# Performance work log

Hardware: AMD Instinct MI355X
Metric: run time of the kernel (lower is better)

The kernel has to match this reference:

```python
import jax, jax.numpy as jnp
import numpy as np

S, B, H = 2048, 1, 1024
N_HEADS = 16
HEAD_DIM = H // N_HEADS
E, K, F = 8, 2, 2048  # experts, top_k, ffn_hidden
EPS = 1e-5


def layernorm(x, w, b):
    mu = jnp.mean(x, axis=-1, keepdims=True)
    var = jnp.mean(jnp.square(x - mu), axis=-1, keepdims=True)
    return (x - mu) * jax.lax.rsqrt(var + EPS) * w + b


def setup_inputs() -> dict:
    key = jax.random.key(0)
    ks = jax.random.split(key, 8)
    std = 0.02
    return {
        "x": jax.random.normal(ks[0], (S, B, H), dtype=jnp.float32),
        "ln1_w": jnp.ones((H,), jnp.float32),
        "ln1_b": jnp.zeros((H,), jnp.float32),
        "in_proj_w": jax.random.normal(ks[1], (3 * H, H), jnp.float32) * std,
        "in_proj_b": jnp.zeros((3 * H,), jnp.float32),
        "out_proj_w": jax.random.normal(ks[2], (H, H), jnp.float32) * std,
        "out_proj_b": jnp.zeros((H,), jnp.float32),
        "ln2_w": jnp.ones((H,), jnp.float32),
        "ln2_b": jnp.zeros((H,), jnp.float32),
        "router_w": jax.random.normal(ks[3], (E, H), jnp.float32) * std,
        "w1": jax.random.normal(ks[4], (E, H, F), jnp.float32) * std,
        "w2": jax.random.normal(ks[5], (E, F, H), jnp.float32) * std,
    }


def reference(x, ln1_w, ln1_b, in_proj_w, in_proj_b, out_proj_w, out_proj_b,
              ln2_w, ln2_b, router_w, w1, w2):
    s, b, h = x.shape
    # ---- causal self-attention (nn.MultiheadAttention math) ----
    hn = layernorm(x, ln1_w, ln1_b)
    qkv = hn @ in_proj_w.T + in_proj_b          # [S,B,3H]
    q, k, v = jnp.split(qkv, 3, axis=-1)
    q = q.reshape(s, b, N_HEADS, HEAD_DIM)
    k = k.reshape(s, b, N_HEADS, HEAD_DIM)
    v = v.reshape(s, b, N_HEADS, HEAD_DIM)
    scores = jnp.einsum('sbnd,tbnd->bnst', q, k) / np.sqrt(HEAD_DIM)
    causal = jnp.tril(jnp.ones((s, s), bool))
    scores = jnp.where(causal[None, None], scores, -jnp.inf)
    probs = jax.nn.softmax(scores, axis=-1)
    attn = jnp.einsum('bnst,tbnd->sbnd', probs, v).reshape(s, b, h)
    attn = attn @ out_proj_w.T + out_proj_b
    x1 = x + attn
    # ---- dMoE FFN: router softmax -> top-k gates -> expert GELU MLP ----
    hn2 = layernorm(x1, ln2_w, ln2_b).reshape(s * b, h)   # tokens [T,H]
    logits = hn2 @ router_w.T                              # [T,E]
    rp = jax.nn.softmax(logits, axis=-1)
    topw, topi = jax.lax.top_k(rp, K)                      # [T,K]
    gates = jnp.sum(jax.nn.one_hot(topi, E, dtype=hn2.dtype) * topw[..., None], axis=1)  # [T,E]
    hmid = jax.nn.gelu(jnp.einsum('th,ehf->tef', hn2, w1), approximate=False)  # [T,E,F]
    y = jnp.einsum('tef,efh->th', hmid * gates[:, :, None], w2)                # [T,H]
    return x1 + y.reshape(s, b, h)
```

## Files before the change

### kernel.cpp

```cpp
#include <hip/hip_runtime.h>

#define SL 2048
#define HID 1024
#define NHEAD 16
#define HD 64
#define NEXP 8
#define FF 2048
#define MAXTILE 40
#define MAXROWS (MAXTILE * 128)
#define CPAD 32

typedef short bf16x8 __attribute__((ext_vector_type(8)));
typedef float f32x4 __attribute__((ext_vector_type(4)));
typedef unsigned u32x4 __attribute__((ext_vector_type(4)));

__device__ __forceinline__ unsigned short f2bf(float f) {
  unsigned u = __builtin_bit_cast(unsigned, f);
  u += 0x7fffu + ((u >> 16) & 1u);
  return (unsigned short)(u >> 16);
}

__device__ __forceinline__ void gload16(const void* g, void* l) {
  __builtin_amdgcn_global_load_lds((const __attribute__((address_space(1))) void*)g,
                                   (__attribute__((address_space(3))) void*)l,
                                   16, 0, 0);
}

__device__ __forceinline__ void xcd_remap(int& bx, int& by) {
  const int nx = gridDim.x;
  const int nwg = nx * gridDim.y;
  const int L = by * nx + bx;
  const int per = nwg >> 3;
  const int Lp = (L & 7) * per + (L >> 3);
  bx = Lp % nx;
  by = Lp / nx;
}

struct TransLds { float Afp[64 * 128]; unsigned Bu[128 * 33]; };

__device__ __forceinline__ void trans_tile(
    int tile, const float* __restrict__ w1, const float* __restrict__ w2,
    unsigned short* __restrict__ w1t, unsigned short* __restrict__ w2t,
    int tid, TransLds* T)
{
  const int m = tile >> 8;
  const int t = tile & 255;
  const float* in;
  unsigned short* out;
  int R, C, r0, c0;
  if (m < 8) {
    in = w1 + (size_t)m * HID * FF;  out = w1t + (size_t)m * HID * FF;
    R = HID; C = FF;  r0 = (t >> 4) * 64;  c0 = (t & 15) * 128;
  } else {
    in = w2 + (size_t)(m - 8) * FF * HID;  out = w2t + (size_t)(m - 8) * FF * HID;
    R = FF; C = HID;  r0 = (t >> 3) * 64;  c0 = (t & 7) * 128;
  }
  const int wv = tid >> 6, ln = tid & 63;
#pragma unroll
  for (int p = 0; p < 8; p++) {
    const int ebase = p * 1024 + wv * 256;
    const int eo = ebase + ln * 4;
    const int r = eo >> 7, c = eo & 127;
    gload16(in + (size_t)(r0 + r) * C + c0 + c, (char*)T->Afp + (size_t)ebase * 4);
  }
  asm volatile("s_waitcnt vmcnt(0)" ::: "memory");
  __syncthreads();
#pragma unroll
  for (int it = 0; it < 16; it++) {
    const int idx = it * 256 + tid;
    const int rp = idx >> 7;
    const int c = idx & 127;
    const float v0 = T->Afp[(2 * rp) * 128 + c];
    const float v1 = T->Afp[(2 * rp + 1) * 128 + c];
    T->Bu[c * 33 + rp] = (unsigned)f2bf(v0) | ((unsigned)f2bf(v1) << 16);
  }
  __syncthreads();
#pragma unroll
  for (int it = 0; it < 8; it++) {
    const int idx = it * 256 + tid;
    const int c = idx >> 4;
    const int r4 = (idx & 15) * 4;
    const unsigned u0 = T->Bu[c * 33 + (r4 >> 1)];
    const unsigned u1 = T->Bu[c * 33 + (r4 >> 1) + 1];
    ushort4 u;
    u.x = (unsigned short)(u0 & 0xffff);
    u.y = (unsigned short)(u0 >> 16);
    u.z = (unsigned short)(u1 & 0xffff);
    u.w = (unsigned short)(u1 >> 16);
    *reinterpret_cast<ushort4*>(&out[(size_t)(c0 + c) * R + r0 + r4]) = u;
  }
}

#define PIPE_WAIT(i, NT)                                                     \
  if ((i) == (NT) - 1)                                                       \
    asm volatile("s_waitcnt vmcnt(0) lgkmcnt(0)" ::: "memory");              \
  else                                                                       \
    asm volatile("s_waitcnt vmcnt(4) lgkmcnt(0)" ::: "memory");              \
  __builtin_amdgcn_s_barrier();

#define GEMM_FRAGS_MFMA(CC)                                                  \
  bf16x8 af[4], bfr[4];                                                      \
  _Pragma("unroll")                                                          \
  for (int mt = 0; mt < 4; mt++)                                             \
    af[mt] = *reinterpret_cast<const bf16x8*>(                               \
        &Asm[CC][(wm + mt * 16 + la) * 32 + lk]);                            \
  _Pragma("unroll")                                                          \
  for (int nt = 0; nt < 4; nt++)                                             \
    bfr[nt] = *reinterpret_cast<const bf16x8*>(                              \
        &Bsm[CC][(wn + nt * 16 + la) * 32 + lk]);                            \
  __builtin_amdgcn_s_setprio(1);                                             \
  _Pragma("unroll")                                                          \
  for (int mt = 0; mt < 4; mt++)                                             \
    _Pragma("unroll")                                                        \
    for (int nt = 0; nt < 4; nt++)                                           \
      acc[mt][nt] =                                                          \
          __builtin_amdgcn_mfma_f32_16x16x32_bf16(af[mt], bfr[nt], acc[mt][nt], 0, 0, 0); \
  __builtin_amdgcn_s_setprio(0);

#define PIPE_ROT()                                                           \
  cc = (cc == 2) ? 0 : cc + 1;                                               \
  cs = (cs == 2) ? 0 : cs + 1;

__global__ __launch_bounds__(256) void qkv_trans_kernel(
    const unsigned short* __restrict__ A, const unsigned short* __restrict__ Bt,
    const float* __restrict__ bias,
    unsigned short* __restrict__ q_out, unsigned short* __restrict__ k_out,
    unsigned short* __restrict__ vt_out,
    const float* __restrict__ w1, const float* __restrict__ w2,
    unsigned short* __restrict__ w1t, unsigned short* __restrict__ w2t)
{
  __shared__ union {
    struct { unsigned short A[3][4096]; unsigned short B[3][4096]; } g;
    TransLds t;
  } sm;
  const int tid = threadIdx.x;

  if (blockIdx.z == 0) {
    unsigned short (*Asm)[4096] = sm.g.A;
    unsigned short (*Bsm)[4096] = sm.g.B;
    int bx = blockIdx.x, by = blockIdx.y;
    xcd_remap(bx, by);
    const int wave = tid >> 6;
    const int lane = tid & 63;
    const int m0 = by * 128;
    const int n0 = bx * 128;
    const int wm = (wave >> 1) * 64;
    const int wn = (wave & 1) * 64;
    const int la = lane & 15;
    const int lk = (lane >> 4) * 8;

    f32x4 acc[4][4] = {};

    const int srow = tid >> 2;
    const int skoff = (tid & 3) * 8;
    const unsigned short* Ag = A + (size_t)(m0 + srow) * HID + skoff;
    const unsigned short* Bg = Bt + (size_t)(n0 + srow) * HID + skoff;

    auto stage = [&](int s, int k0) {
      gload16(Ag + k0, &Asm[s][wave * 512]);
      gload16(Ag + (size_t)64 * HID + k0, &Asm[s][2048 + wave * 512]);
      gload16(Bg + k0, &Bsm[s][wave * 512]);
      gload16(Bg + (size_t)64 * HID + k0, &Bsm[s][2048 + wave * 512]);
    };

    stage(0, 0);
    stage(1, 32);
    const int NT = HID >> 5;
    int cc = 0, cs = 2;
    for (int i = 0; i < NT; ++i) {
      PIPE_WAIT(i, NT)
      if (i + 2 < NT) stage(cs, (i + 2) << 5);
      GEMM_FRAGS_MFMA(cc)
      PIPE_ROT()
    }

    const int lg = lane >> 4;
#pragma unroll
    for (int mt = 0; mt < 4; mt++) {
#pragma unroll
      for (int nt = 0; nt < 4; nt++) {
#pragma unroll
        for (int r = 0; r < 4; r++) {
          const int row = m0 + wm + mt * 16 + lg * 4 + r;
          const int col = n0 + wn + nt * 16 + la;
          float v = acc[mt][nt][r] + bias[col];
          const int hh = (col & 1023) >> 6;
          const int dd = col & 63;
          const unsigned short bv = f2bf(v);
          if (col < 1024)
            q_out[(size_t)hh * SL * HD + (size_t)row * HD + dd] = bv;
          else if (col < 2048)
            k_out[(size_t)hh * SL * HD + (size_t)row * HD + dd] = bv;
          else
            vt_out[(size_t)hh * HD * SL + (size_t)dd * SL + row] = bv;
        }
      }
    }
  } else {
    const int id = blockIdx.y * 24 + blockIdx.x;
    const int tile = 512 + ((int)blockIdx.z - 1) * 384 + id;
    trans_tile(tile, w1, w2, w1t, w2t, tid, &sm.t);
  }
}

__global__ __launch_bounds__(256) void gemm_bt2(
    const unsigned short* __restrict__ A, const unsigned short* __restrict__ Bt,
    float* __restrict__ outf,
    const float* __restrict__ w1, const float* __restrict__ w2,
    unsigned short* __restrict__ w1t, unsigned short* __restrict__ w2t)
{
  __shared__ union {
    struct { unsigned short A[3][4096]; unsigned short B[3][4096]; } g;
    TransLds t;
  } sm;
  const int tid = threadIdx.x;

  if (blockIdx.z >= 2) {
    const int id = blockIdx.y * 8 + blockIdx.x;
    const int tile = 3200 + ((int)blockIdx.z - 2) * 128 + id;
    trans_tile(tile, w1, w2, w1t, w2t, tid, &sm.t);
    return;
  }

  unsigned short (*Asm)[4096] = sm.g.A;
  unsigned short (*Bsm)[4096] = sm.g.B;
  int bx = blockIdx.x, by = blockIdx.y;
  xcd_remap(bx, by);
  const int wave = tid >> 6;
  const int lane = tid & 63;
  const int m0 = by * 128;
  const int n0 = bx * 128;
  const int koff = blockIdx.z * (HID / 2);
  const int wm = (wave >> 1) * 64;
  const int wn = (wave & 1) * 64;
  const int la = lane & 15;
  const int lk = (lane >> 4) * 8;

  f32x4 acc[4][4] = {};

  const int srow = tid >> 2;
  const int skoff = (tid & 3) * 8;
  const unsigned short* Ag = A + (size_t)(m0 + srow) * HID + koff + skoff;
  const unsigned short* Bg = Bt + (size_t)(n0 + srow) * HID + koff + skoff;

  auto stage = [&](int s, int k0) {
    gload16(Ag + k0, &Asm[s][wave * 512]);
    gload16(Ag + (size_t)64 * HID + k0, &Asm[s][2048 + wave * 512]);
    gload16(Bg + k0, &Bsm[s][wave * 512]);
    gload16(Bg + (size_t)64 * HID + k0, &Bsm[s][2048 + wave * 512]);
  };

  stage(0, 0);
  stage(1, 32);
  const int NT = (HID / 2) >> 5;
  int cc = 0, cs = 2;
  for (int i = 0; i < NT; ++i) {
    PIPE_WAIT(i, NT)
    if (i + 2 < NT) stage(cs, (i + 2) << 5);
    GEMM_FRAGS_MFMA(cc)
    PIPE_ROT()
  }

  const int lg = lane >> 4;
#pragma unroll
  for (int mt = 0; mt < 4; mt++) {
#pragma unroll
    for (int nt = 0; nt < 4; nt++) {
#pragma unroll
      for (int r = 0; r < 4; r++) {
        const int row = m0 + wm + mt * 16 + lg * 4 + r;
        const int col = n0 + wn + nt * 16 + la;
        outf[(size_t)blockIdx.z * SL * HID + (size_t)row * HID + col] = acc[mt][nt][r];
      }
    }
  }
}

__global__ __launch_bounds__(256) void gemm_moe1(
    const unsigned short* __restrict__ A, const unsigned short* __restrict__ w1t,
    const int* __restrict__ perm, const float* __restrict__ gateg,
    const int* __restrict__ texp, const int* __restrict__ trow,
    unsigned short* __restrict__ hmidg)
{
  __shared__ unsigned short Asm[3][128 * 32];
  __shared__ unsigned short Bsm[3][128 * 32];
  int bx = blockIdx.x, by = blockIdx.y;
  xcd_remap(bx, by);
  const int e = texp[by];
  if (e < 0) return;
  const int row0 = trow[by];
  const int tid = threadIdx.x;
  const int wave = tid >> 6;
  const int lane = tid & 63;
  const int n0 = bx * 128;
  const int wm = (wave >> 1) * 64;
  const int wn = (wave & 1) * 64;
  const int la = lane & 15;
  const int lk = (lane >> 4) * 8;
  f32x4 acc[4][4] = {};

  const int srow = tid >> 2;
  const int skoff = (tid & 3) * 8;
  const int p0 = perm[row0 + srow];
  const int p1 = perm[row0 + 64 + srow];
  const unsigned short* Ag0 = A + (size_t)(p0 < 0 ? 0 : (p0 >> 1)) * HID + skoff;
  const unsigned short* Ag1 = A + (size_t)(p1 < 0 ? 0 : (p1 >> 1)) * HID + skoff;
  const unsigned short* Bg = w1t + (size_t)e * HID * FF + (size_t)(n0 + srow) * HID + skoff;

  auto stage = [&](int s, int k0) {
    gload16(Ag0 + k0, &Asm[s][wave * 512]);
    gload16(Ag1 + k0, &Asm[s][2048 + wave * 512]);
    gload16(Bg + k0, &Bsm[s][wave * 512]);
    gload16(Bg + (size_t)64 * HID + k0, &Bsm[s][2048 + wave * 512]);
  };

  stage(0, 0);
  stage(1, 32);
  const int NT = HID >> 5;
  int cc = 0, cs = 2;
  for (int i = 0; i < NT; ++i) {
    PIPE_WAIT(i, NT)
    if (i + 2 < NT) stage(cs, (i + 2) << 5);
    GEMM_FRAGS_MFMA(cc)
    PIPE_ROT()
  }

  const int lg = lane >> 4;
#pragma unroll
  for (int mt = 0; mt < 4; mt++) {
    float gr[4];
#pragma unroll
    for (int r = 0; r < 4; r++) gr[r] = gateg[row0 + wm + mt * 16 + lg * 4 + r];
#pragma unroll
    for (int nt = 0; nt < 4; nt++) {
#pragma unroll
      for (int r = 0; r < 4; r++) {
        const int grow = row0 + wm + mt * 16 + lg * 4 + r;
        const int col = n0 + wn + nt * 16 + la;
        const float v = acc[mt][nt][r];
        const float g = 0.5f * v * (1.0f + erff(v * 0.70710678118f));
        hmidg[(size_t)grow * FF + col] = f2bf(g * gr[r]);
      }
    }
  }
}

__global__ __launch_bounds__(256) void gemm_moe2(
    const unsigned short* __restrict__ A, const unsigned short* __restrict__ w2t,
    const int* __restrict__ perm,
    const int* __restrict__ texp, const int* __restrict__ trow,
    float* __restrict__ ybuf)
{
  __shared__ unsigned short Asm[3][128 * 32];
  __shared__ unsigned short Bsm[3][128 * 32];
  int bx = blockIdx.x, by = blockIdx.y;
  xcd_remap(bx, by);
  const int e = texp[by];
  if (e < 0) return;
  const int row0 = trow[by];
  const int tid = threadIdx.x;
  const int wave = tid >> 6;
  const int lane = tid & 63;
  const int n0 = bx * 128;
  const int koff = blockIdx.z * (FF / 2);
  const int wm = (wave >> 1) * 64;
  const int wn = (wave & 1) * 64;
  const int la = lane & 15;
  const int lk = (lane >> 4) * 8;
  f32x4 acc[4][4] = {};

  const int srow = tid >> 2;
  const int skoff = (tid & 3) * 8;
  const unsigned short* Ag = A + (size_t)(row0 + srow) * FF + koff + skoff;
  const unsigned short* Bg = w2t + (size_t)e * FF * HID + (size_t)(n0 + srow) * FF + koff + skoff;

  auto stage = [&](int s, int k0) {
    gload16(Ag + k0, &Asm[s][wave * 512]);
    gload16(Ag + (size_t)64 * FF + k0, &Asm[s][2048 + wave * 512]);
    gload16(Bg + k0, &Bsm[s][wave * 512]);
    gload16(Bg + (size_t)64 * FF + k0, &Bsm[s][2048 + wave * 512]);
  };

  stage(0, 0);
  stage(1, 32);
  const int NT = (FF / 2) >> 5;
  int cc = 0, cs = 2;
  for (int i = 0; i < NT; ++i) {
    PIPE_WAIT(i, NT)
    if (i + 2 < NT) stage(cs, (i + 2) << 5);
    GEMM_FRAGS_MFMA(cc)
    PIPE_ROT()
  }

  const int lg = lane >> 4;
#pragma unroll
  for (int mt = 0; mt < 4; mt++) {
    int pr[4];
#pragma unroll
    for (int r = 0; r < 4; r++) pr[r] = perm[row0 + wm + mt * 16 + lg * 4 + r];
#pragma unroll
    for (int nt = 0; nt < 4; nt++) {
#pragma unroll
      for (int r = 0; r < 4; r++) {
        const int p = pr[r];
        if (p >= 0) {
          const int col = n0 + wn + nt * 16 + la;
          ybuf[(size_t)(blockIdx.z * 2 + (p & 1)) * SL * HID + (size_t)(p >> 1) * HID + col] =
              acc[mt][nt][r];
        }
      }
    }
  }
}

__global__ __launch_bounds__(256) void ln_conv_kernel(
    const float* __restrict__ x, const float* __restrict__ w, const float* __restrict__ b,
    unsigned short* __restrict__ ob,
    const float4* __restrict__ cva, const float4* __restrict__ cvb,
    ushort4* __restrict__ coa, ushort4* __restrict__ cob,
    const float* __restrict__ w1, const float* __restrict__ w2,
    unsigned short* __restrict__ w1t, unsigned short* __restrict__ w2t)
{
  __shared__ union { struct { float ps[4], pq[4]; } l; TransLds t; } sm;
  const int tid = threadIdx.x;
  if ((int)blockIdx.x < SL) {
    const int row = blockIdx.x;
    const float4 v = *reinterpret_cast<const float4*>(&x[(size_t)row * HID + tid * 4]);
    float s = v.x + v.y + v.z + v.w;
    float q = v.x * v.x + v.y * v.y + v.z * v.z + v.w * v.w;
    for (int off = 32; off > 0; off >>= 1) {
      s += __shfl_down(s, off);
      q += __shfl_down(q, off);
    }
    const int wave = tid >> 6, lane = tid & 63;
    if (lane == 0) { sm.l.ps[wave] = s; sm.l.pq[wave] = q; }
    __syncthreads();
    s = sm.l.ps[0] + sm.l.ps[1] + sm.l.ps[2] + sm.l.ps[3];
    q = sm.l.pq[0] + sm.l.pq[1] + sm.l.pq[2] + sm.l.pq[3];
    const float mu = s * (1.0f / HID);
    const float inv = rsqrtf(q * (1.0f / HID) - mu * mu + 1e-5f);
    const int i = tid * 4;
    const float4 wv = *reinterpret_cast<const float4*>(&w[i]);
    const float4 bv = *reinterpret_cast<const float4*>(&b[i]);
    ushort4 u;
    u.x = f2bf((v.x - mu) * inv * wv.x + bv.x);
    u.y = f2bf((v.y - mu) * inv * wv.y + bv.y);
    u.z = f2bf((v.z - mu) * inv * wv.z + bv.z);
    u.w = f2bf((v.w - mu) * inv * wv.w + bv.w);
    *reinterpret_cast<ushort4*>(&ob[(size_t)row * HID + i]) = u;
  } else if ((int)blockIdx.x < SL + 512) {
    const int NA = 3 * HID * HID / 4, NB = HID * HID / 4;
    for (int i = ((int)blockIdx.x - SL) * 256 + tid; i < NA + NB; i += 512 * 256) {
      if (i < NA) {
        const float4 v = cva[i];
        ushort4 u; u.x = f2bf(v.x); u.y = f2bf(v.y); u.z = f2bf(v.z); u.w = f2bf(v.w);
        coa[i] = u;
      } else {
        const float4 v = cvb[i - NA];
        ushort4 u; u.x = f2bf(v.x); u.y = f2bf(v.y); u.z = f2bf(v.z); u.w = f2bf(v.w);
        cob[i - NA] = u;
      }
    }
  } else {
    const int tile = (int)blockIdx.x - SL - 512;
    trans_tile(tile, w1, w2, w1t, w2t, tid, &sm.t);
  }
}

__global__ __launch_bounds__(256) void combine_ln(
    const float4* __restrict__ x, const float* __restrict__ bias,
    const float4* __restrict__ p0, const float4* __restrict__ p1,
    float4* __restrict__ x1,
    const float* __restrict__ w, const float* __restrict__ b,
    unsigned short* __restrict__ ob,
    const float* __restrict__ rw,
    int* __restrict__ ti, float* __restrict__ tg, int* __restrict__ cnt)
{
  __shared__ float ps[4], pq[4];
  __shared__ float rsm[4][8];
  const int row = blockIdx.x;
  const int tid = threadIdx.x;
  const int i4 = row * 256 + tid;
  const int i = tid * 4;
  const float4 bv0 = *reinterpret_cast<const float4*>(&bias[i]);
  const float4 a = x[i4], c = p0[i4], d = p1[i4];
  float4 v;
  v.x = a.x + bv0.x + c.x + d.x;
  v.y = a.y + bv0.y + c.y + d.y;
  v.z = a.z + bv0.z + c.z + d.z;
  v.w = a.w + bv0.w + c.w + d.w;
  x1[i4] = v;
  float s = v.x + v.y + v.z + v.w;
  float q = v.x * v.x + v.y * v.y + v.z * v.z + v.w * v.w;
  for (int off = 32; off > 0; off >>= 1) {
    s += __shfl_down(s, off);
    q += __shfl_down(q, off);
  }
  const int wave = tid >> 6, lane = tid & 63;
  if (lane == 0) { ps[wave] = s; pq[wave] = q; }
  __syncthreads();
  s = ps[0] + ps[1] + ps[2] + ps[3];
  q = pq[0] + pq[1] + pq[2] + pq[3];
  const float mu = s * (1.0f / HID);
  const float inv = rsqrtf(q * (1.0f / HID) - mu * mu + 1e-5f);
  const float4 wv = *reinterpret_cast<const float4*>(&w[i]);
  const float4 bv = *reinterpret_cast<const float4*>(&b[i]);
  const float o0 = (v.x - mu) * inv * wv.x + bv.x;
  const float o1 = (v.y - mu) * inv * wv.y + bv.y;
  const float o2 = (v.z - mu) * inv * wv.z + bv.z;
  const float o3 = (v.w - mu) * inv * wv.w + bv.w;
  ushort4 u; u.x = f2bf(o0); u.y = f2bf(o1); u.z = f2bf(o2); u.w = f2bf(o3);
  *reinterpret_cast<ushort4*>(&ob[(size_t)row * HID + i]) = u;

  float pl[NEXP];
#pragma unroll
  for (int e = 0; e < NEXP; e++) {
    const float4 rv = *reinterpret_cast<const float4*>(&rw[e * HID + i]);
    pl[e] = o0 * rv.x + o1 * rv.y + o2 * rv.z + o3 * rv.w;
  }
#pragma unroll
  for (int e = 0; e < NEXP; e++) {
    pl[e] += __shfl_xor(pl[e], 32);
    pl[e] += __shfl_xor(pl[e], 16);
    pl[e] += __shfl_xor(pl[e], 8);
    pl[e] += __shfl_xor(pl[e], 4);
    pl[e] += __shfl_xor(pl[e], 2);
    pl[e] += __shfl_xor(pl[e], 1);
  }
  if (lane == 0) {
#pragma unroll
    for (int e = 0; e < NEXP; e++) rsm[wave][e] = pl[e];
  }
  __syncthreads();
  if (tid == 0) {
    float lgt[NEXP];
#pragma unroll
    for (int e = 0; e < NEXP; e++)
      lgt[e] = rsm[0][e] + rsm[1][e] + rsm[2][e] + rsm[3][e];
    float mx = lgt[0];
#pragma unroll
    for (int e = 1; e < NEXP; e++) mx = fmaxf(mx, lgt[e]);
    float Z = 0.f;
    float pexp[NEXP];
#pragma unroll
    for (int e = 0; e < NEXP; e++) { pexp[e] = expf(lgt[e] - mx); Z += pexp[e]; }
    const float invZ = 1.f / Z;
    int i1 = 0;
#pragma unroll
    for (int e = 1; e < NEXP; e++) if (pexp[e] > pexp[i1]) i1 = e;
    int i2 = (i1 == 0) ? 1 : 0;
#pragma unroll
    for (int e = 0; e < NEXP; e++) if (e != i1 && pexp[e] > pexp[i2]) i2 = e;
    ti[2 * row] = i1; ti[2 * row + 1] = i2;
    tg[2 * row] = pexp[i1] * invZ; tg[2 * row + 1] = pexp[i2] * invZ;
    atomicAdd(&cnt[i1 * CPAD], 1);
    atomicAdd(&cnt[i2 * CPAD], 1);
  }
}

__global__ __launch_bounds__(256) void scan_build_kernel(
    const int* __restrict__ cnt, const int* __restrict__ ti, const float* __restrict__ tg,
    int* __restrict__ texp, int* __restrict__ trow,
    int* __restrict__ perm, float* __restrict__ gateg)
{
  __shared__ int poff[NEXP];
  __shared__ int lfill[NEXP];
  const int tid = threadIdx.x;
  if (tid == 0) {
    int off = 0, nt = 0;
    for (int e = 0; e < NEXP; e++) {
      poff[e] = off;
      const int c = cnt[e * CPAD];
      const int ntl = (c + 127) >> 7;
      for (int i = 0; i < ntl; i++) { texp[nt] = e; trow[nt] = off + i * 128; nt++; }
      off += ntl * 128;
    }
    for (int i = nt; i < MAXTILE; i++) { texp[i] = -1; trow[i] = 0; }
  }
  if (tid < NEXP) lfill[tid] = 0;
  __syncthreads();
  for (int t = tid; t < SL; t += 256) {
#pragma unroll
    for (int s2 = 0; s2 < 2; s2++) {
      const int e = ti[2 * t + s2];
      const int l = atomicAdd(&lfill[e], 1);
      const int pos = poff[e] + l;
      perm[pos] = 2 * t + s2;
      gateg[pos] = tg[2 * t + s2];
    }
  }
}

__global__ __launch_bounds__(256) void final_add(
    const float4* __restrict__ x1, const float4* __restrict__ y0,
    const float4* __restrict__ y1, const float4* __restrict__ y2,
    const float4* __restrict__ y3, float4* __restrict__ out)
{
  const int i = blockIdx.x * 256 + threadIdx.x;
  const float4 a = x1[i], b = y0[i], c = y1[i], d = y2[i], e = y3[i];
  float4 o;
  o.x = a.x + b.x + c.x + d.x + e.x;
  o.y = a.y + b.y + c.y + d.y + e.y;
  o.z = a.z + b.z + c.z + d.z + e.z;
  o.w = a.w + b.w + c.w + d.w + e.w;
  out[i] = o;
}

#define SC2 0.1803368801111204f
#define PPITCH 20
__global__ __launch_bounds__(512) void attn_kernel(
    const unsigned short* __restrict__ qb, const unsigned short* __restrict__ kb,
    const unsigned short* __restrict__ vtb, unsigned short* __restrict__ attn)
{
  const int h = blockIdx.y;
  const int tid = threadIdx.x;
  const int wave = tid >> 6, lane = tid & 63;
  const int grp = wave >> 2;
  const int w4 = wave & 3;
  const int la = lane & 15, lg = lane >> 4;
  const int la7 = la & 7;
  __shared__ unsigned short Kt[2][2][64 * 64];
  __shared__ unsigned short Vt[2][2][64 * 64];
  __shared__ unsigned plds[8 * 32 * PPITCH];
  const unsigned short* qh = qb + (size_t)h * SL * HD;
  const unsigned short* kh = kb + (size_t)h * SL * HD;
  const unsigned short* vh = vtb + (size_t)h * HD * SL;
  unsigned* pu = &plds[wave * 32 * PPITCH];

  const int sr_lo = w4 * 8 + (lane >> 3);
  const int ss = lane & 7;

  auto stageKV = [&](int t, int buf) {
    const int kvb = t * 64;
#pragma unroll
    for (int j = 0; j < 2; j++) {
      const int row = j * 32 + sr_lo;
      const int s = ss ^ (row & 7);
      gload16(kh + (size_t)(kvb + row) * HD + s * 8, &Kt[grp][buf][j * 2048 + w4 * 512]);
      gload16(vh + (size_t)row * SL + kvb + s * 8, &Vt[grp][buf][j * 2048 + w4 * 512]);
    }
  };

  for (int half = 0; half < 2; half++) {
    const int qt = half ? (31 - blockIdx.x) : blockIdx.x;
    const int m0 = qt * 64 + w4 * 16;
    const int T = qt + 1;
    const int S = (T + 1) >> 1;
    const int q = m0 + la;

    bf16x8 aq0 = *reinterpret_cast<const bf16x8*>(&qh[(size_t)(m0 + la) * HD + lg * 8]);
    bf16x8 aq1 = *reinterpret_cast<const bf16x8*>(&qh[(size_t)(m0 + la) * HD + 32 + lg * 8]);

    f32x4 oacc[4] = {};
    float mrun = -1e30f, lrun = 0.f;

    if (grp < T) stageKV(grp, 0);
    __syncthreads();
    int cur = 0;

    for (int s = 0; s < S; s++) {
      const int tmy = 2 * s + grp;
      if (tmy + 2 < T) stageKV(tmy + 2, cur ^ 1);
      if (tmy < T) {
        const int kv0 = tmy * 64;
        const unsigned short* Kb = Kt[grp][cur];
        const unsigned short* Vb = Vt[grp][cur];

        f32x4 sac[4] = {};
        __builtin_amdgcn_s_setprio(1);
#pragma unroll
        for (int nt = 0; nt < 4; nt++) {
          const int row = nt * 16 + la;
          bf16x8 b0 = *reinterpret_cast<const bf16x8*>(&Kb[row * 64 + ((lg ^ la7) << 3)]);
          bf16x8 b1 = *reinterpret_cast<const bf16x8*>(&Kb[row * 64 + (((4 + lg) ^ la7) << 3)]);
          sac[nt] = __builtin_amdgcn_mfma_f32_16x16x32_bf16(b0, aq0, sac[nt], 0, 0, 0);
          sac[nt] = __builtin_amdgcn_mfma_f32_16x16x32_bf16(b1, aq1, sac[nt], 0, 0, 0);
        }
        __builtin_amdgcn_s_setprio(0);
        float sv[4][4];
        const bool diag = (tmy == qt);
#pragma unroll
        for (int nt = 0; nt < 4; nt++)
#pragma unroll
          for (int r = 0; r < 4; r++) {
            float xs = sac[nt][r] * SC2;
            if (diag && (kv0 + nt * 16 + lg * 4 + r) > q) xs = -1e30f;
            sv[nt][r] = xs;
          }
        float pm = fmaxf(fmaxf(sv[0][0], sv[0][1]), fmaxf(sv[0][2], sv[0][3]));
#pragma unroll
        for (int nt = 1; nt < 4; nt++)
          pm = fmaxf(pm, fmaxf(fmaxf(sv[nt][0], sv[nt][1]), fmaxf(sv[nt][2], sv[nt][3])));
        pm = fmaxf(pm, __shfl_xor(pm, 16));
        pm = fmaxf(pm, __shfl_xor(pm, 32));
        const float mn = fmaxf(mrun, pm);
        float rs = 0.f;
#pragma unroll
        for (int nt = 0; nt < 4; nt++)
#pragma unroll
          for (int r = 0; r < 4; r++) {
            const float pe = exp2f(sv[nt][r] - mn);
            sv[nt][r] = pe;
            rs += pe;
          }
        rs += __shfl_xor(rs, 16);
        rs += __shfl_xor(rs, 32);
        if (__ballot(pm > mrun) != 0ULL) {
          const float al = exp2f(mrun - mn);
#pragma unroll
          for (int dt = 0; dt < 4; dt++)
#pragma unroll
            for (int r = 0; r < 4; r++) oacc[dt][r] *= al;
          lrun = lrun * al + rs;
          mrun = mn;
        } else {
          lrun += rs;
        }
#pragma unroll
        for (int nt = 0; nt < 4; nt++)
#pragma unroll
          for (int rp = 0; rp < 2; rp++) {
            unsigned pk;
            asm("v_cvt_pk_bf16_f32 %0, %1, %2"
                : "=v"(pk) : "v"(sv[nt][rp * 2]), "v"(sv[nt][rp * 2 + 1]));
            pu[(nt * 8 + lg * 2 + rp) * PPITCH + la] = pk;
          }
        asm volatile("s_waitcnt lgkmcnt(0)" ::: "memory");
        __builtin_amdgcn_sched_barrier(0);
        u32x4 w0, w1;
#pragma unroll
        for (int jj = 0; jj < 4; jj++) {
          w0[jj] = pu[(lg * 4 + jj) * PPITCH + la];
          w1[jj] = pu[(16 + lg * 4 + jj) * PPITCH + la];
        }
        const bf16x8 pa0 = __builtin_bit_cast(bf16x8, w0);
        const bf16x8 pa1 = __builtin_bit_cast(bf16x8, w1);
        __builtin_amdgcn_s_setprio(1);
#pragma unroll
        for (int dt = 0; dt < 4; dt++) {
          const int row = dt * 16 + la;
          bf16x8 v0 = *reinterpret_cast<const bf16x8*>(&Vb[row * 64 + ((lg ^ la7) << 3)]);
          bf16x8 v1 = *reinterpret_cast<const bf16x8*>(&Vb[row * 64 + (((4 + lg) ^ la7) << 3)]);
          oacc[dt] = __builtin_amdgcn_mfma_f32_16x16x32_bf16(v0, pa0, oacc[dt], 0, 0, 0);
          oacc[dt] = __builtin_amdgcn_mfma_f32_16x16x32_bf16(v1, pa1, oacc[dt], 0, 0, 0);
        }
        __builtin_amdgcn_s_setprio(0);
      }
      __syncthreads();
      cur ^= 1;
    }

    float* xb = (float*)&Kt[0][0][0];
    float* mlb = (float*)&Vt[0][0][0];
    if (grp == 1) {
#pragma unroll
      for (int dt = 0; dt < 4; dt++)
#pragma unroll
        for (int r = 0; r < 4; r++)
          xb[w4 * 1024 + (dt * 16 + lg * 4 + r) * 16 + la] = oacc[dt][r];
      if (lg == 0) {
        mlb[w4 * 32 + la * 2] = mrun;
        mlb[w4 * 32 + la * 2 + 1] = lrun;
      }
    }
    __syncthreads();
    if (grp == 0) {
      const float m1 = mlb[w4 * 32 + la * 2];
      const float l1 = mlb[w4 * 32 + la * 2 + 1];
      const float mm = fmaxf(mrun, m1);
      const float a0 = exp2f(mrun - mm);
      const float a1 = exp2f(m1 - mm);
      const float linv = 1.0f / (lrun * a0 + l1 * a1);
#pragma unroll
      for (int dt = 0; dt < 4; dt++) {
        ushort4 u;
        float o0 = (oacc[dt][0] * a0 + xb[w4 * 1024 + (dt * 16 + lg * 4 + 0) * 16 + la] * a1) * linv;
        float o1 = (oacc[dt][1] * a0 + xb[w4 * 1024 + (dt * 16 + lg * 4 + 1) * 16 + la] * a1) * linv;
        float o2 = (oacc[dt][2] * a0 + xb[w4 * 1024 + (dt * 16 + lg * 4 + 2) * 16 + la] * a1) * linv;
        float o3 = (oacc[dt][3] * a0 + xb[w4 * 1024 + (dt * 16 + lg * 4 + 3) * 16 + la] * a1) * linv;
        u.x = f2bf(o0); u.y = f2bf(o1); u.z = f2bf(o2); u.w = f2bf(o3);
        *reinterpret_cast<ushort4*>(&attn[(size_t)q * HID + h * HD + dt * 16 + lg * 4]) = u;
      }
    }
    __syncthreads();
  }
}

extern "C" void kernel_launch(void* const* d_in, const int* in_sizes, int n_in,
                              void* d_out, int out_size, void* d_ws, size_t ws_size,
                              hipStream_t stream)
{
  const float* x          = (const float*)d_in[0];
  const float* ln1_w      = (const float*)d_in[1];
  const float* ln1_b      = (const float*)d_in[2];
  const float* in_proj_w  = (const float*)d_in[3];
  const float* in_proj_b  = (const float*)d_in[4];
  const float* out_proj_w = (const float*)d_in[5];
  const float* out_proj_b = (const float*)d_in[6];
  const float* ln2_w      = (const float*)d_in[7];
  const float* ln2_b      = (const float*)d_in[8];
  const float* router_w   = (const float*)d_in[9];
  const float* w1         = (const float*)d_in[10];
  const float* w2         = (const float*)d_in[11];
  float* out = (float*)d_out;

  char* ws = (char*)d_ws;
  size_t off = 0;
  auto alloc = [&](size_t bytes) -> void* {
    void* p = ws + off;
    off += (bytes + 255) & ~(size_t)255;
    return p;
  };
  unsigned short* hn_b   = (unsigned short*)alloc((size_t)SL * HID * 2);
  unsigned short* ipw_b  = (unsigned short*)alloc((size_t)3 * HID * HID * 2);
  unsigned short* opw_b  = (unsigned short*)alloc((size_t)HID * HID * 2);
  unsigned short* qb     = (unsigned short*)alloc((size_t)SL * HID * 2);
  unsigned short* kb     = (unsigned short*)alloc((size_t)SL * HID * 2);
  unsigned short* vtb    = (unsigned short*)alloc((size_t)SL * HID * 2);
  unsigned short* attn_b = (unsigned short*)alloc((size_t)SL * HID * 2);
  float*          x1     = (float*)alloc((size_t)SL * HID * 4);
  float*          pbuf   = (float*)alloc((size_t)2 * SL * HID * 4);
  unsigned short* hn2_b  = (unsigned short*)alloc((size_t)SL * HID * 2);
  unsigned short* w1t    = (unsigned short*)alloc((size_t)NEXP * HID * FF * 2);
  unsigned short* w2t    = (unsigned short*)alloc((size_t)NEXP * HID * FF * 2);
  unsigned short* hmidg  = (unsigned short*)alloc((size_t)MAXROWS * FF * 2);
  float*          ybuf   = (float*)alloc((size_t)4 * SL * HID * 4);
  int*            ti     = (int*)alloc((size_t)SL * 2 * 4);
  float*          tg     = (float*)alloc((size_t)SL * 2 * 4);
  int*            perm   = (int*)alloc((size_t)MAXROWS * 4);
  float*          gateg  = (float*)alloc((size_t)MAXROWS * 4);
  int*            cnt    = (int*)alloc(NEXP * CPAD * 4);
  int*            poff   = (int*)alloc(64 * 4);
  int*            texp   = (int*)alloc(64 * 4);
  int*            trow   = (int*)alloc(64 * 4);
  (void)poff;

  const dim3 blk(256);

  hipMemsetAsync(cnt, 0, NEXP * CPAD * 4, stream);
  hipMemsetAsync(perm, 0xFF, (size_t)MAXROWS * 4, stream);
  hipMemsetAsync(gateg, 0, (size_t)MAXROWS * 4, stream);

  ln_conv_kernel<<<SL + 1024, blk, 0, stream>>>(
      x, ln1_w, ln1_b, hn_b,
      (const float4*)in_proj_w, (const float4*)out_proj_w,
      (ushort4*)ipw_b, (ushort4*)opw_b,
      w1, w2, w1t, w2t);

  qkv_trans_kernel<<<dim3(3 * HID / 128, SL / 128, 8), blk, 0, stream>>>(
      hn_b, ipw_b, in_proj_b, qb, kb, vtb, w1, w2, w1t, w2t);

  attn_kernel<<<dim3(16, NHEAD), dim3(512), 0, stream>>>(qb, kb, vtb, attn_b);

  gemm_bt2<<<dim3(HID / 128, SL / 128, 9), blk, 0, stream>>>(
      attn_b, opw_b, pbuf, w1, w2, w1t, w2t);

  combine_ln<<<SL, blk, 0, stream>>>(
      (const float4*)x, out_proj_b, (const float4*)pbuf,
      (const float4*)(pbuf + (size_t)SL * HID), (float4*)x1,
      ln2_w, ln2_b, hn2_b,
      router_w, ti, tg, cnt);

  scan_build_kernel<<<1, blk, 0, stream>>>(cnt, ti, tg, texp, trow, perm, gateg);

  gemm_moe1<<<dim3(FF / 128, MAXTILE), blk, 0, stream>>>(
      hn2_b, w1t, perm, gateg, texp, trow, hmidg);
  gemm_moe2<<<dim3(HID / 128, MAXTILE, 2), blk, 0, stream>>>(
      hmidg, w2t, perm, texp, trow, ybuf);

  final_add<<<SL * HID / 1024, blk, 0, stream>>>(
      (const float4*)x1, (const float4*)ybuf,
      (const float4*)(ybuf + (size_t)SL * HID),
      (const float4*)(ybuf + (size_t)2 * SL * HID),
      (const float4*)(ybuf + (size_t)3 * SL * HID),
      (float4*)out);
}
```

Before: 244.8 us.

## Fuse scan into combine_ln via last-block pattern and atomically accumulate MoE output

```diff
diff --git a/kernel.cpp b/kernel.cpp
--- a/kernel.cpp
+++ b/kernel.cpp
@@ -349,7 +349,7 @@
     const unsigned short* __restrict__ A, const unsigned short* __restrict__ w2t,
     const int* __restrict__ perm,
     const int* __restrict__ texp, const int* __restrict__ trow,
-    float* __restrict__ ybuf)
+    float* __restrict__ outbuf)
 {
   __shared__ unsigned short Asm[3][128 * 32];
   __shared__ unsigned short Bsm[3][128 * 32];
@@ -405,8 +405,7 @@
         const int p = pr[r];
         if (p >= 0) {
           const int col = n0 + wn + nt * 16 + la;
-          ybuf[(size_t)(blockIdx.z * 2 + (p & 1)) * SL * HID + (size_t)(p >> 1) * HID + col] =
-              acc[mt][nt][r];
+          atomicAdd(&outbuf[(size_t)(p >> 1) * HID + col], acc[mt][nt][r]);
         }
       }
     }
@@ -470,14 +469,20 @@
 __global__ __launch_bounds__(256) void combine_ln(
     const float4* __restrict__ x, const float* __restrict__ bias,
     const float4* __restrict__ p0, const float4* __restrict__ p1,
-    float4* __restrict__ x1,
+    float4* __restrict__ outbuf,
     const float* __restrict__ w, const float* __restrict__ b,
     unsigned short* __restrict__ ob,
     const float* __restrict__ rw,
-    int* __restrict__ ti, float* __restrict__ tg, int* __restrict__ cnt)
+    int* __restrict__ ti, float* __restrict__ tg, int* __restrict__ cnt,
+    int* __restrict__ donecnt,
+    int* __restrict__ texp, int* __restrict__ trow,
+    int* __restrict__ perm, float* __restrict__ gateg)
 {
   __shared__ float ps[4], pq[4];
   __shared__ float rsm[4][8];
+  __shared__ int poff[NEXP];
+  __shared__ int lfill[NEXP];
+  __shared__ int lastflag;
   const int row = blockIdx.x;
   const int tid = threadIdx.x;
   const int i4 = row * 256 + tid;
@@ -489,7 +494,7 @@
   v.y = a.y + bv0.y + c.y + d.y;
   v.z = a.z + bv0.z + c.z + d.z;
   v.w = a.w + bv0.w + c.w + d.w;
-  x1[i4] = v;
+  outbuf[i4] = v;
   float s = v.x + v.y + v.z + v.w;
   float q = v.x * v.x + v.y * v.y + v.z * v.z + v.w * v.w;
   for (int off = 32; off > 0; off >>= 1) {
@@ -556,26 +561,25 @@
     atomicAdd(&cnt[i1 * CPAD], 1);
     atomicAdd(&cnt[i2 * CPAD], 1);
   }
-}
-
-__global__ __launch_bounds__(256) void scan_build_kernel(
-    const int* __restrict__ cnt, const int* __restrict__ ti, const float* __restrict__ tg,
-    int* __restrict__ texp, int* __restrict__ trow,
-    int* __restrict__ perm, float* __restrict__ gateg)
-{
-  __shared__ int poff[NEXP];
-  __shared__ int lfill[NEXP];
-  const int tid = threadIdx.x;
+
+  __threadfence();
+  if (tid == 0) {
+    const int dcnt = atomicAdd(donecnt, 1);
+    lastflag = (dcnt == (int)gridDim.x - 1);
+  }
+  __syncthreads();
+  if (!lastflag) return;
+  __threadfence();
   if (tid == 0) {
     int off = 0, nt = 0;
     for (int e = 0; e < NEXP; e++) {
       poff[e] = off;
-      const int c = cnt[e * CPAD];
-      const int ntl = (c + 127) >> 7;
-      for (int i = 0; i < ntl; i++) { texp[nt] = e; trow[nt] = off + i * 128; nt++; }
+      const int ce = atomicAdd(&cnt[e * CPAD], 0);
+      const int ntl = (ce + 127) >> 7;
+      for (int t2 = 0; t2 < ntl; t2++) { texp[nt] = e; trow[nt] = off + t2 * 128; nt++; }
       off += ntl * 128;
     }
-    for (int i = nt; i < MAXTILE; i++) { texp[i] = -1; trow[i] = 0; }
+    for (int t2 = nt; t2 < MAXTILE; t2++) { texp[t2] = -1; trow[t2] = 0; }
   }
   if (tid < NEXP) lfill[tid] = 0;
   __syncthreads();
@@ -589,21 +593,6 @@
       gateg[pos] = tg[2 * t + s2];
     }
   }
-}
-
-__global__ __launch_bounds__(256) void final_add(
-    const float4* __restrict__ x1, const float4* __restrict__ y0,
-    const float4* __restrict__ y1, const float4* __restrict__ y2,
-    const float4* __restrict__ y3, float4* __restrict__ out)
-{
-  const int i = blockIdx.x * 256 + threadIdx.x;
-  const float4 a = x1[i], b = y0[i], c = y1[i], d = y2[i], e = y3[i];
-  float4 o;
-  o.x = a.x + b.x + c.x + d.x + e.x;
-  o.y = a.y + b.y + c.y + d.y + e.y;
-  o.z = a.z + b.z + c.z + d.z + e.z;
-  o.w = a.w + b.w + c.w + d.w + e.w;
-  out[i] = o;
 }
 
 #define SC2 0.1803368801111204f
@@ -818,26 +807,23 @@
   unsigned short* kb     = (unsigned short*)alloc((size_t)SL * HID * 2);
   unsigned short* vtb    = (unsigned short*)alloc((size_t)SL * HID * 2);
   unsigned short* attn_b = (unsigned short*)alloc((size_t)SL * HID * 2);
-  float*          x1     = (float*)alloc((size_t)SL * HID * 4);
   float*          pbuf   = (float*)alloc((size_t)2 * SL * HID * 4);
   unsigned short* hn2_b  = (unsigned short*)alloc((size_t)SL * HID * 2);
   unsigned short* w1t    = (unsigned short*)alloc((size_t)NEXP * HID * FF * 2);
   unsigned short* w2t    = (unsigned short*)alloc((size_t)NEXP * HID * FF * 2);
   unsigned short* hmidg  = (unsigned short*)alloc((size_t)MAXROWS * FF * 2);
-  float*          ybuf   = (float*)alloc((size_t)4 * SL * HID * 4);
   int*            ti     = (int*)alloc((size_t)SL * 2 * 4);
   float*          tg     = (float*)alloc((size_t)SL * 2 * 4);
   int*            perm   = (int*)alloc((size_t)MAXROWS * 4);
   float*          gateg  = (float*)alloc((size_t)MAXROWS * 4);
-  int*            cnt    = (int*)alloc(NEXP * CPAD * 4);
-  int*            poff   = (int*)alloc(64 * 4);
+  int*            cnt    = (int*)alloc((NEXP + 1) * CPAD * 4);
+  int*            donecnt = cnt + NEXP * CPAD;
   int*            texp   = (int*)alloc(64 * 4);
   int*            trow   = (int*)alloc(64 * 4);
-  (void)poff;
 
   const dim3 blk(256);
 
-  hipMemsetAsync(cnt, 0, NEXP * CPAD * 4, stream);
+  hipMemsetAsync(cnt, 0, (NEXP + 1) * CPAD * 4, stream);
   hipMemsetAsync(perm, 0xFF, (size_t)MAXROWS * 4, stream);
   hipMemsetAsync(gateg, 0, (size_t)MAXROWS * 4, stream);
 
@@ -857,21 +843,12 @@
 
   combine_ln<<<SL, blk, 0, stream>>>(
       (const float4*)x, out_proj_b, (const float4*)pbuf,
-      (const float4*)(pbuf + (size_t)SL * HID), (float4*)x1,
+      (const float4*)(pbuf + (size_t)SL * HID), (float4*)out,
       ln2_w, ln2_b, hn2_b,
-      router_w, ti, tg, cnt);
-
-  scan_build_kernel<<<1, blk, 0, stream>>>(cnt, ti, tg, texp, trow, perm, gateg);
+      router_w, ti, tg, cnt, donecnt, texp, trow, perm, gateg);
 
   gemm_moe1<<<dim3(FF / 128, MAXTILE), blk, 0, stream>>>(
       hn2_b, w1t, perm, gateg, texp, trow, hmidg);
   gemm_moe2<<<dim3(HID / 128, MAXTILE, 2), blk, 0, stream>>>(
-      hmidg, w2t, perm, texp, trow, ybuf);
-
-  final_add<<<SL * HID / 1024, blk, 0, stream>>>(
-      (const float4*)x1, (const float4*)ybuf,
-      (const float4*)(ybuf + (size_t)SL * HID),
-      (const float4*)(ybuf + (size_t)2 * SL * HID),
-      (const float4*)(ybuf + (size_t)3 * SL * HID),
-      (float4*)out);
-}
+      hmidg, w2t, perm, texp, trow, out);
+}
```

Result: slower. 438.2 us (+79.0%).

## Move part of expert weight transpose work into attention kernel grid

Applied to the files above, without the earlier changes.

```diff
diff --git a/kernel.cpp b/kernel.cpp
--- a/kernel.cpp
+++ b/kernel.cpp
@@ -38,16 +38,13 @@
 
 struct TransLds { float Afp[64 * 128]; unsigned Bu[128 * 33]; };
 
-__device__ __forceinline__ void trans_tile(
+__device__ __forceinline__ void trans_geom(
     int tile, const float* __restrict__ w1, const float* __restrict__ w2,
     unsigned short* __restrict__ w1t, unsigned short* __restrict__ w2t,
-    int tid, TransLds* T)
+    const float*& in, unsigned short*& out, int& R, int& C, int& r0, int& c0)
 {
   const int m = tile >> 8;
   const int t = tile & 255;
-  const float* in;
-  unsigned short* out;
-  int R, C, r0, c0;
   if (m < 8) {
     in = w1 + (size_t)m * HID * FF;  out = w1t + (size_t)m * HID * FF;
     R = HID; C = FF;  r0 = (t >> 4) * 64;  c0 = (t & 15) * 128;
@@ -55,6 +52,15 @@
     in = w2 + (size_t)(m - 8) * FF * HID;  out = w2t + (size_t)(m - 8) * FF * HID;
     R = FF; C = HID;  r0 = (t >> 3) * 64;  c0 = (t & 7) * 128;
   }
+}
+
+__device__ __forceinline__ void trans_tile(
+    int tile, const float* __restrict__ w1, const float* __restrict__ w2,
+    unsigned short* __restrict__ w1t, unsigned short* __restrict__ w2t,
+    int tid, TransLds* T)
+{
+  const float* in; unsigned short* out; int R, C, r0, c0;
+  trans_geom(tile, w1, w2, w1t, w2t, in, out, R, C, r0, c0);
   const int wv = tid >> 6, ln = tid & 63;
 #pragma unroll
   for (int p = 0; p < 8; p++) {
@@ -78,6 +84,49 @@
 #pragma unroll
   for (int it = 0; it < 8; it++) {
     const int idx = it * 256 + tid;
+    const int c = idx >> 4;
+    const int r4 = (idx & 15) * 4;
+    const unsigned u0 = T->Bu[c * 33 + (r4 >> 1)];
+    const unsigned u1 = T->Bu[c * 33 + (r4 >> 1) + 1];
+    ushort4 u;
+    u.x = (unsigned short)(u0 & 0xffff);
+    u.y = (unsigned short)(u0 >> 16);
+    u.z = (unsigned short)(u1 & 0xffff);
+    u.w = (unsigned short)(u1 >> 16);
+    *reinterpret_cast<ushort4*>(&out[(size_t)(c0 + c) * R + r0 + r4]) = u;
+  }
+}
+
+__device__ __forceinline__ void trans_tile512(
+    int tile, const float* __restrict__ w1, const float* __restrict__ w2,
+    unsigned short* __restrict__ w1t, unsigned short* __restrict__ w2t,
+    int tid, TransLds* T)
+{
+  const float* in; unsigned short* out; int R, C, r0, c0;
+  trans_geom(tile, w1, w2, w1t, w2t, in, out, R, C, r0, c0);
+  const int wv = tid >> 6, ln = tid & 63;
+#pragma unroll
+  for (int p = 0; p < 4; p++) {
+    const int ebase = p * 2048 + wv * 256;
+    const int eo = ebase + ln * 4;
+    const int r = eo >> 7, c = eo & 127;
+    gload16(in + (size_t)(r0 + r) * C + c0 + c, (char*)T->Afp + (size_t)ebase * 4);
+  }
+  asm volatile("s_waitcnt vmcnt(0)" ::: "memory");
+  __syncthreads();
+#pragma unroll
+  for (int it = 0; it < 8; it++) {
+    const int idx = it * 512 + tid;
+    const int rp = idx >> 7;
+    const int c = idx & 127;
+    const float v0 = T->Afp[(2 * rp) * 128 + c];
+    const float v1 = T->Afp[(2 * rp + 1) * 128 + c];
+    T->Bu[c * 33 + rp] = (unsigned)f2bf(v0) | ((unsigned)f2bf(v1) << 16);
+  }
+  __syncthreads();
+#pragma unroll
+  for (int it = 0; it < 4; it++) {
+    const int idx = it * 512 + tid;
     const int c = idx >> 4;
     const int r4 = (idx & 15) * 4;
     const unsigned u0 = T->Bu[c * 33 + (r4 >> 1)];
@@ -198,7 +247,8 @@
     }
   } else {
     const int id = blockIdx.y * 24 + blockIdx.x;
-    const int tile = 512 + ((int)blockIdx.z - 1) * 384 + id;
+    const int tile = 1536 + ((int)blockIdx.z - 1) * 384 + id;
+    if (tile >= 3200) return;
     trans_tile(tile, w1, w2, w1t, w2t, tid, &sm.t);
   }
 }
@@ -607,25 +657,40 @@
 }
 
 #define SC2 0.1803368801111204f
-#define PPITCH 20
+#define PPITCH 16
 __global__ __launch_bounds__(512) void attn_kernel(
     const unsigned short* __restrict__ qb, const unsigned short* __restrict__ kb,
-    const unsigned short* __restrict__ vtb, unsigned short* __restrict__ attn)
-{
+    const unsigned short* __restrict__ vtb, unsigned short* __restrict__ attn,
+    const float* __restrict__ w1, const float* __restrict__ w2,
+    unsigned short* __restrict__ w1t, unsigned short* __restrict__ w2t)
+{
+  __shared__ union {
+    struct {
+      unsigned short Kt[2][2][64 * 64];
+      unsigned short Vt[2][2][64 * 64];
+      unsigned plds[8 * 32 * PPITCH];
+    } a;
+    TransLds t;
+  } sm;
+  const int tid = threadIdx.x;
+
+  if (blockIdx.z > 0) {
+    const int id = blockIdx.y * 16 + blockIdx.x;
+    const int tile = 512 + ((int)blockIdx.z - 1) * 256 + id;
+    trans_tile512(tile, w1, w2, w1t, w2t, tid, &sm.t);
+    return;
+  }
+
   const int h = blockIdx.y;
-  const int tid = threadIdx.x;
   const int wave = tid >> 6, lane = tid & 63;
   const int grp = wave >> 2;
   const int w4 = wave & 3;
   const int la = lane & 15, lg = lane >> 4;
   const int la7 = la & 7;
-  __shared__ unsigned short Kt[2][2][64 * 64];
-  __shared__ unsigned short Vt[2][2][64 * 64];
-  __shared__ unsigned plds[8 * 32 * PPITCH];
   const unsigned short* qh = qb + (size_t)h * SL * HD;
   const unsigned short* kh = kb + (size_t)h * SL * HD;
   const unsigned short* vh = vtb + (size_t)h * HD * SL;
-  unsigned* pu = &plds[wave * 32 * PPITCH];
+  unsigned* pu = &sm.a.plds[wave * 32 * PPITCH];
 
   const int sr_lo = w4 * 8 + (lane >> 3);
   const int ss = lane & 7;
@@ -636,8 +701,8 @@
     for (int j = 0; j < 2; j++) {
       const int row = j * 32 + sr_lo;
       const int s = ss ^ (row & 7);
-      gload16(kh + (size_t)(kvb + row) * HD + s * 8, &Kt[grp][buf][j * 2048 + w4 * 512]);
-      gload16(vh + (size_t)row * SL + kvb + s * 8, &Vt[grp][buf][j * 2048 + w4 * 512]);
+      gload16(kh + (size_t)(kvb + row) * HD + s * 8, &sm.a.Kt[grp][buf][j * 2048 + w4 * 512]);
+      gload16(vh + (size_t)row * SL + kvb + s * 8, &sm.a.Vt[grp][buf][j * 2048 + w4 * 512]);
     }
   };
 
@@ -663,8 +728,8 @@
       if (tmy + 2 < T) stageKV(tmy + 2, cur ^ 1);
       if (tmy < T) {
         const int kv0 = tmy * 64;
-        const unsigned short* Kb = Kt[grp][cur];
-        const unsigned short* Vb = Vt[grp][cur];
+        const unsigned short* Kb = sm.a.Kt[grp][cur];
+        const unsigned short* Vb = sm.a.Vt[grp][cur];
 
         f32x4 sac[4] = {};
         __builtin_amdgcn_s_setprio(1);
@@ -727,14 +792,14 @@
           }
         asm volatile("s_waitcnt lgkmcnt(0)" ::: "memory");
         __builtin_amdgcn_sched_barrier(0);
-        u32x4 w0, w1;
+        u32x4 w0, w1v;
 #pragma unroll
         for (int jj = 0; jj < 4; jj++) {
           w0[jj] = pu[(lg * 4 + jj) * PPITCH + la];
-          w1[jj] = pu[(16 + lg * 4 + jj) * PPITCH + la];
+          w1v[jj] = pu[(16 + lg * 4 + jj) * PPITCH + la];
         }
         const bf16x8 pa0 = __builtin_bit_cast(bf16x8, w0);
-        const bf16x8 pa1 = __builtin_bit_cast(bf16x8, w1);
+        const bf16x8 pa1 = __builtin_bit_cast(bf16x8, w1v);
         __builtin_amdgcn_s_setprio(1);
 #pragma unroll
         for (int dt = 0; dt < 4; dt++) {
@@ -750,8 +815,8 @@
       cur ^= 1;
     }
 
-    float* xb = (float*)&Kt[0][0][0];
-    float* mlb = (float*)&Vt[0][0][0];
+    float* xb = (float*)&sm.a.Kt[0][0][0];
+    float* mlb = (float*)&sm.a.Vt[0][0][0];
     if (grp == 1) {
 #pragma unroll
       for (int dt = 0; dt < 4; dt++)
@@ -830,10 +895,8 @@
   int*            perm   = (int*)alloc((size_t)MAXROWS * 4);
   float*          gateg  = (float*)alloc((size_t)MAXROWS * 4);
   int*            cnt    = (int*)alloc(NEXP * CPAD * 4);
-  int*            poff   = (int*)alloc(64 * 4);
   int*            texp   = (int*)alloc(64 * 4);
   int*            trow   = (int*)alloc(64 * 4);
-  (void)poff;
 
   const dim3 blk(256);
 
@@ -847,10 +910,11 @@
       (ushort4*)ipw_b, (ushort4*)opw_b,
       w1, w2, w1t, w2t);
 
-  qkv_trans_kernel<<<dim3(3 * HID / 128, SL / 128, 8), blk, 0, stream>>>(
+  qkv_trans_kernel<<<dim3(3 * HID / 128, SL / 128, 6), blk, 0, stream>>>(
       hn_b, ipw_b, in_proj_b, qb, kb, vtb, w1, w2, w1t, w2t);
 
-  attn_kernel<<<dim3(16, NHEAD), dim3(512), 0, stream>>>(qb, kb, vtb, attn_b);
+  attn_kernel<<<dim3(16, NHEAD, 5), dim3(512), 0, stream>>>(
+      qb, kb, vtb, attn_b, w1, w2, w1t, w2t);
 
   gemm_bt2<<<dim3(HID / 128, SL / 128, 9), blk, 0, stream>>>(
       attn_b, opw_b, pbuf, w1, w2, w1t, w2t);
```

Result: faster. 234.7 us (-4.1%).
